# Optimization experiments

Hardware: AMD Instinct MI355X
Metric: run time of the kernel (lower is better)

## Reference

```python
import jax, jax.numpy as jnp
import numpy as np

NBITS = 1
GROUP_SIZE = 64
OUT_F = 4096
IN_F = 4096


def setup_inputs() -> dict:
    key = jax.random.key(0)
    k1, k2, k3, k4, k5 = jax.random.split(key, 5)
    x = jax.random.normal(k1, (8192, IN_F), dtype=jnp.float32)
    # packed 1-bit weights: 8 bits per byte, stored as int32 in [0,256)
    W_packed = jax.random.randint(k2, (OUT_F, IN_F // 8), 0, 256, dtype=jnp.int32)
    n_groups = OUT_F * IN_F // GROUP_SIZE
    scale = jax.random.uniform(k3, (n_groups, 1), dtype=jnp.float32) * 0.02 + 0.005
    zero = jax.random.normal(k4, (n_groups, 1), dtype=jnp.float32) * 0.5
    bias = jax.random.normal(k5, (OUT_F,), dtype=jnp.float32) * 0.02
    return {"x": x, "W_packed": W_packed, "scale": scale, "zero": zero, "bias": bias}


def _unpack_1bit(W_packed):
    # (out, in//8) int -> (out, in) float bits, bit 0 first within each byte
    bits = (W_packed[..., None] >> jnp.arange(8, dtype=jnp.int32)) & 1  # (out, in//8, 8)
    return bits.reshape(W_packed.shape[0], -1).astype(jnp.float32)      # (out, in)


def _dequantise(W_packed, scale, zero):
    W_q = _unpack_1bit(W_packed)                       # (out, in)
    W_grouped = W_q.reshape(-1, GROUP_SIZE)            # (n_groups, group_size), axis=1 grouping
    W_hat = (W_grouped - zero) * scale                 # per-group affine dequant
    return W_hat.reshape(OUT_F, IN_F)


def reference(x, W_packed, scale, zero, bias):
    W_hat = _dequantise(W_packed, scale, zero)
    # F.linear: x @ W_hat.T + bias
    return jnp.dot(x, W_hat.T) + bias
```

## Files before the change

### kernel.cpp

```cpp
#include <hip/hip_runtime.h>
#include <hip/hip_bf16.h>

#define IN_F   4096
#define OUT_F  4096
#define BK     64
#define NTILES (IN_F / BK)

typedef __bf16 bf16;
typedef __attribute__((ext_vector_type(8)))  __bf16 bf16x8;
typedef __attribute__((ext_vector_type(4)))  __bf16 bf16x4;
typedef __attribute__((ext_vector_type(4)))  float  floatx4;

__global__ __launch_bounds__(256) void prep_kernel(
    const float* __restrict__ x,  bf16* __restrict__ xb,
    const int* __restrict__ Wp,   const float* __restrict__ scale,
    const float* __restrict__ zero, bf16* __restrict__ Wb,
    int nx8, int nw)
{
    const int tid0   = (int)blockIdx.x * 256 + (int)threadIdx.x;
    const int stride = (int)gridDim.x * 256;

    for (int i = tid0; i < nx8; i += stride) {
        const float4 v0 = ((const float4*)x)[2 * (size_t)i];
        const float4 v1 = ((const float4*)x)[2 * (size_t)i + 1];
        bf16x8 b;
        b[0] = (bf16)v0.x; b[1] = (bf16)v0.y; b[2] = (bf16)v0.z; b[3] = (bf16)v0.w;
        b[4] = (bf16)v1.x; b[5] = (bf16)v1.y; b[6] = (bf16)v1.z; b[7] = (bf16)v1.w;
        ((bf16x8*)xb)[i] = b;
    }

    for (int i = tid0; i < nw; i += stride) {
        const int b = i & 511;
        const int g = ((i >> 9) << 6) + (b >> 3);
        const float sc = scale[g];
        const float zp = zero[g];
        const bf16 hi = (bf16)((1.0f - zp) * sc);
        const bf16 lo = (bf16)((0.0f - zp) * sc);
        const int v = Wp[i];
        bf16x8 w;
#pragma unroll
        for (int j = 0; j < 8; ++j) w[j] = ((v >> j) & 1) ? hi : lo;
        *(bf16x8*)&Wb[(size_t)i * 8] = w;
    }
}

__device__ __forceinline__ void gload_lds16(const void* g, void* l) {
    __builtin_amdgcn_global_load_lds(
        (const __attribute__((address_space(1))) unsigned int*)g,
        (__attribute__((address_space(3))) unsigned int*)l, 16, 0, 0);
}

#define CFENCE asm volatile("" ::: "memory")
#define SBAR() do { CFENCE; __builtin_amdgcn_s_barrier(); CFENCE; } while (0)
#define WAIT_LGKM0 asm volatile("s_waitcnt lgkmcnt(0)" ::: "memory")

#define STAGE(src, ldsTile, q, row0, kti) do {                                 \
    const int r_  = (q) * 64 + wave * 8 + srow;                                \
    const int gu_ = sun ^ (r_ & 7);                                            \
    gload_lds16((src) + (size_t)((row0) + r_) * IN_F + (kti) * BK + gu_ * 8,   \
                (ldsTile) + ((q) * 64 + wave * 8) * BK);                       \
} while (0)

#define LDFRAG(tile, row, u) \
    (*(const bf16x8*)((tile) + (row) * BK + (((u) ^ ((row) & 7)) << 3)))

#define LOAD_A(tile, MS)                                                       \
    _Pragma("unroll")                                                          \
    for (int i = 0; i < 4; ++i)                                                \
        _Pragma("unroll")                                                      \
        for (int ks = 0; ks < 2; ++ks)                                         \
            af[i][ks] = LDFRAG((tile), wm * 128 + (MS) * 64 + i * 16 + l15,    \
                               ks * 4 + l4);

#define LOAD_B_TO(dst, tile, NS)                                               \
    _Pragma("unroll")                                                          \
    for (int j = 0; j < 2; ++j)                                                \
        _Pragma("unroll")                                                      \
        for (int ks = 0; ks < 2; ++ks)                                         \
            dst[j][ks] = LDFRAG((tile), wn * 64 + (NS) * 32 + j * 16 + l15,    \
                                ks * 4 + l4);

#define MFMA_QUAD(AI, BJ, BFR)                                                 \
    __builtin_amdgcn_s_setprio(1);                                             \
    _Pragma("unroll")                                                          \
    for (int i = 0; i < 4; ++i)                                                \
        _Pragma("unroll")                                                      \
        for (int j = 0; j < 2; ++j)                                            \
            _Pragma("unroll")                                                  \
            for (int ks = 0; ks < 2; ++ks)                                     \
                acc[(AI) + i][(BJ) + j] =                                      \
                    __builtin_amdgcn_mfma_f32_16x16x32_bf16(                   \
                        af[i][ks], BFR[j][ks], acc[(AI) + i][(BJ) + j], 0, 0, 0); \
    __builtin_amdgcn_s_setprio(0);

__global__ __launch_bounds__(512, 2) void gemm256_8phase_kernel(
    const bf16* __restrict__ A,
    const bf16* __restrict__ B,
    const float* __restrict__ bias,
    float* __restrict__ out)
{
    __shared__ __align__(16) bf16 as_[2][256 * BK];
    __shared__ __align__(16) bf16 bs_[2][256 * BK];

    const int t    = threadIdx.x;
    const int lane = t & 63;
    const int wave = t >> 6;
    const int wm   = wave >> 2;
    const int wn   = wave & 3;
    const int l15  = lane & 15;
    const int l4   = lane >> 4;
    const int srow = lane >> 3;
    const int sun  = lane & 7;

    const int nwg = (int)gridDim.x;
    const int cpx = nwg >> 3;
    const int wg  = ((int)blockIdx.x & 7) * cpx + ((int)blockIdx.x >> 3);
    const int n0  = (wg & 15) * 256;
    const int m0  = (wg >> 4) * 256;

    floatx4 acc[8][4];
#pragma unroll
    for (int f = 0; f < 8; ++f)
#pragma unroll
        for (int g = 0; g < 4; ++g) acc[f][g] = (floatx4){0.f, 0.f, 0.f, 0.f};

#pragma unroll
    for (int q = 0; q < 4; ++q) STAGE(A, &as_[0][0], q, m0, 0);
#pragma unroll
    for (int q = 0; q < 4; ++q) STAGE(B, &bs_[0][0], q, n0, 0);
    STAGE(A, &as_[1][0], 0, m0, 1);
    STAGE(A, &as_[1][0], 2, m0, 1);
    asm volatile("s_waitcnt vmcnt(2)" ::: "memory");
    SBAR();

    bf16x8 af[4][2], bf0[2][2], bf1[2][2];

    for (int kt = 0; kt < NTILES; ++kt) {
        bf16* const At = &as_[kt & 1][0];
        bf16* const Bt = &bs_[kt & 1][0];
        bf16* const An = &as_[(kt & 1) ^ 1][0];
        bf16* const Bn = &bs_[(kt & 1) ^ 1][0];
        const int s1 = (kt + 1 < NTILES);
        const int s2 = (kt + 2 < NTILES);

        LOAD_A(At, 0);
        LOAD_B_TO(bf0, Bt, 0);
        if (s1) { STAGE(B, Bn, 0, n0, kt + 1); STAGE(B, Bn, 1, n0, kt + 1); }
        SBAR(); WAIT_LGKM0;
        MFMA_QUAD(0, 0, bf0);
        SBAR();

        LOAD_B_TO(bf1, Bt, 1);
        if (s1) { STAGE(B, Bn, 2, n0, kt + 1); STAGE(B, Bn, 3, n0, kt + 1); }
        SBAR(); WAIT_LGKM0;
        MFMA_QUAD(0, 2, bf1);
        if (s1) { asm volatile("s_waitcnt vmcnt(6)" ::: "memory"); }
        else    { asm volatile("s_waitcnt vmcnt(0)" ::: "memory"); }
        SBAR();

        LOAD_A(At, 1);
        if (s1) { STAGE(A, An, 1, m0, kt + 1); STAGE(A, An, 3, m0, kt + 1); }
        SBAR(); WAIT_LGKM0;
        MFMA_QUAD(4, 0, bf0);
        SBAR();

        if (s2) { STAGE(A, At, 0, m0, kt + 2); STAGE(A, At, 2, m0, kt + 2); }
        MFMA_QUAD(4, 2, bf1);
        if (s2) { asm volatile("s_waitcnt vmcnt(4)" ::: "memory"); }
        else    { asm volatile("s_waitcnt vmcnt(2)" ::: "memory"); }
        SBAR();
    }

#pragma unroll
    for (int g = 0; g < 4; ++g) {
        const int col = n0 + wn * 64 + g * 16 + l15;
        const float bv = bias[col];
#pragma unroll
        for (int f = 0; f < 8; ++f) {
            const int row = m0 + wm * 128 + f * 16 + l4 * 4;
#pragma unroll
            for (int r = 0; r < 4; ++r)
                out[(size_t)(row + r) * OUT_F + col] = acc[f][g][r] + bv;
        }
    }
}

#define SA 72
#define SB 72
__global__ __launch_bounds__(256) void hqq_gemm_fused_kernel(
    const float* __restrict__ x, const int* __restrict__ Wp,
    const float* __restrict__ scale, const float* __restrict__ zero,
    const float* __restrict__ bias, float* __restrict__ out)
{
    __shared__ __align__(16) bf16 asmem[128 * SA];
    __shared__ __align__(16) bf16 bsmem[128 * SB];
    const int t = threadIdx.x, lane = t & 63, wave = t >> 6;
    const int lane16 = lane & 15, kq = lane >> 4;
    const int wm = wave >> 1, wn = wave & 1;
    const int n0 = blockIdx.x * 128, m0 = blockIdx.y * 128;
    floatx4 acc[4][4];
#pragma unroll
    for (int i = 0; i < 4; ++i)
#pragma unroll
        for (int j = 0; j < 4; ++j) acc[i][j] = (floatx4){0.f, 0.f, 0.f, 0.f};
    const int a_col4 = t & 15, a_row0 = t >> 4;
    const int b_nl = t >> 1, b_half = t & 1;
    for (int kt = 0; kt < IN_F / 64; ++kt) {
        const float* xp = x + (size_t)(m0 + a_row0) * IN_F + kt * 64 + a_col4 * 4;
#pragma unroll
        for (int p = 0; p < 8; ++p) {
            float4 v = *(const float4*)(xp + (size_t)(p * 16) * IN_F);
            bf16x4 b = { (bf16)v.x, (bf16)v.y, (bf16)v.z, (bf16)v.w };
            *(bf16x4*)&asmem[(a_row0 + p * 16) * SA + a_col4 * 4] = b;
        }
        {
            const int4 v = *(const int4*)(Wp + (size_t)(n0 + b_nl) * (IN_F / 8)
                                          + kt * 8 + b_half * 4);
            const int g = (n0 + b_nl) * (IN_F / 64) + kt;
            const float sc = scale[g], zp = zero[g];
            const bf16 hi = (bf16)((1.0f - zp) * sc), lo = (bf16)(0.0f - zp * sc);
            const int vals[4] = {v.x, v.y, v.z, v.w};
#pragma unroll
            for (int e = 0; e < 4; ++e) {
                bf16x8 w;
#pragma unroll
                for (int j = 0; j < 8; ++j) w[j] = ((vals[e] >> j) & 1) ? hi : lo;
                *(bf16x8*)&bsmem[b_nl * SB + b_half * 32 + e * 8] = w;
            }
        }
        __syncthreads();
#pragma unroll
        for (int ks = 0; ks < 2; ++ks) {
            bf16x8 af[4], bfr[4];
#pragma unroll
            for (int i = 0; i < 4; ++i)
                af[i] = *(const bf16x8*)&asmem[(wm * 64 + i * 16 + lane16) * SA + ks * 32 + kq * 8];
#pragma unroll
            for (int j = 0; j < 4; ++j)
                bfr[j] = *(const bf16x8*)&bsmem[(wn * 64 + j * 16 + lane16) * SB + ks * 32 + kq * 8];
#pragma unroll
            for (int i = 0; i < 4; ++i)
#pragma unroll
                for (int j = 0; j < 4; ++j)
                    acc[i][j] = __builtin_amdgcn_mfma_f32_16x16x32_bf16(af[i], bfr[j], acc[i][j], 0, 0, 0);
        }
        __syncthreads();
    }
#pragma unroll
    for (int j = 0; j < 4; ++j) {
        const int col = n0 + wn * 64 + j * 16 + lane16;
        const float bv = bias[col];
#pragma unroll
        for (int i = 0; i < 4; ++i) {
            const int row = m0 + wm * 64 + i * 16 + kq * 4;
#pragma unroll
            for (int r = 0; r < 4; ++r)
                out[(size_t)(row + r) * OUT_F + col] = acc[i][j][r] + bv;
        }
    }
}

extern "C" void kernel_launch(void* const* d_in, const int* in_sizes, int n_in,
                              void* d_out, int out_size, void* d_ws, size_t ws_size,
                              hipStream_t stream) {
    const float* x     = (const float*)d_in[0];
    const int*   Wp    = (const int*)d_in[1];
    const float* scale = (const float*)d_in[2];
    const float* zero  = (const float*)d_in[3];
    const float* bias  = (const float*)d_in[4];
    float*       out   = (float*)d_out;

    const int M = in_sizes[0] / IN_F;
    const size_t need = (size_t)M * IN_F * 2 + (size_t)OUT_F * IN_F * 2;

    if (ws_size >= need && (M % 256) == 0) {
        bf16* xb = (bf16*)d_ws;
        bf16* Wb = (bf16*)((char*)d_ws + (size_t)M * IN_F * 2);

        const int nx8 = M * IN_F / 8;
        const int nw  = OUT_F * (IN_F / 8);
        prep_kernel<<<2048, 256, 0, stream>>>(x, xb, Wp, scale, zero, Wb, nx8, nw);

        gemm256_8phase_kernel<<<dim3((OUT_F / 256) * (M / 256)), 512, 0, stream>>>(
            xb, Wb, bias, out);
    } else {
        dim3 grid(OUT_F / 128, M / 128);
        hqq_gemm_fused_kernel<<<grid, 256, 0, stream>>>(x, Wp, scale, zero, bias, out);
    }
}
```

Measured before the change: 475.5 us.

## Fuse x conversion and weight dequant into the 256x256 GEMM main loop

```diff
diff --git a/kernel.cpp b/kernel.cpp
--- a/kernel.cpp
+++ b/kernel.cpp
@@ -11,54 +11,61 @@
 typedef __attribute__((ext_vector_type(4)))  __bf16 bf16x4;
 typedef __attribute__((ext_vector_type(4)))  float  floatx4;
 
-__global__ __launch_bounds__(256) void prep_kernel(
-    const float* __restrict__ x,  bf16* __restrict__ xb,
-    const int* __restrict__ Wp,   const float* __restrict__ scale,
-    const float* __restrict__ zero, bf16* __restrict__ Wb,
-    int nx8, int nw)
-{
-    const int tid0   = (int)blockIdx.x * 256 + (int)threadIdx.x;
-    const int stride = (int)gridDim.x * 256;
-
-    for (int i = tid0; i < nx8; i += stride) {
-        const float4 v0 = ((const float4*)x)[2 * (size_t)i];
-        const float4 v1 = ((const float4*)x)[2 * (size_t)i + 1];
-        bf16x8 b;
-        b[0] = (bf16)v0.x; b[1] = (bf16)v0.y; b[2] = (bf16)v0.z; b[3] = (bf16)v0.w;
-        b[4] = (bf16)v1.x; b[5] = (bf16)v1.y; b[6] = (bf16)v1.z; b[7] = (bf16)v1.w;
-        ((bf16x8*)xb)[i] = b;
-    }
-
-    for (int i = tid0; i < nw; i += stride) {
-        const int b = i & 511;
-        const int g = ((i >> 9) << 6) + (b >> 3);
-        const float sc = scale[g];
-        const float zp = zero[g];
-        const bf16 hi = (bf16)((1.0f - zp) * sc);
-        const bf16 lo = (bf16)((0.0f - zp) * sc);
-        const int v = Wp[i];
-        bf16x8 w;
-#pragma unroll
-        for (int j = 0; j < 8; ++j) w[j] = ((v >> j) & 1) ? hi : lo;
-        *(bf16x8*)&Wb[(size_t)i * 8] = w;
-    }
-}
-
-__device__ __forceinline__ void gload_lds16(const void* g, void* l) {
-    __builtin_amdgcn_global_load_lds(
-        (const __attribute__((address_space(1))) unsigned int*)g,
-        (__attribute__((address_space(3))) unsigned int*)l, 16, 0, 0);
-}
 
 #define CFENCE asm volatile("" ::: "memory")
 #define SBAR() do { CFENCE; __builtin_amdgcn_s_barrier(); CFENCE; } while (0)
 #define WAIT_LGKM0 asm volatile("s_waitcnt lgkmcnt(0)" ::: "memory")
 
-#define STAGE(src, ldsTile, q, row0, kti) do {                                 \
-    const int r_  = (q) * 64 + wave * 8 + srow;                                \
-    const int gu_ = sun ^ (r_ & 7);                                            \
-    gload_lds16((src) + (size_t)((row0) + r_) * IN_F + (kti) * BK + gu_ * 8,   \
-                (ldsTile) + ((q) * 64 + wave * 8) * BK);                       \
+#define LD_A2(nm, qa, qb, kti) do {                                            \
+    const int rA_ = (qa) * 64 + wave * 8 + srow;                               \
+    const int rB_ = (qb) * 64 + wave * 8 + srow;                               \
+    const float* pA_ = X + (size_t)(m0 + rA_) * IN_F + (kti) * BK + gu * 8;    \
+    const float* pB_ = X + (size_t)(m0 + rB_) * IN_F + (kti) * BK + gu * 8;    \
+    nm##_00 = *(const float4*)pA_;  nm##_01 = *(const float4*)(pA_ + 4);       \
+    nm##_10 = *(const float4*)pB_;  nm##_11 = *(const float4*)(pB_ + 4);       \
+} while (0)
+
+#define WR_A2(nm, qa, qb, buf) do {                                            \
+    const int rA_ = (qa) * 64 + wave * 8 + srow;                               \
+    const int rB_ = (qb) * 64 + wave * 8 + srow;                               \
+    bf16x8 vA_, vB_;                                                           \
+    vA_[0]=(bf16)nm##_00.x; vA_[1]=(bf16)nm##_00.y;                            \
+    vA_[2]=(bf16)nm##_00.z; vA_[3]=(bf16)nm##_00.w;                            \
+    vA_[4]=(bf16)nm##_01.x; vA_[5]=(bf16)nm##_01.y;                            \
+    vA_[6]=(bf16)nm##_01.z; vA_[7]=(bf16)nm##_01.w;                            \
+    vB_[0]=(bf16)nm##_10.x; vB_[1]=(bf16)nm##_10.y;                            \
+    vB_[2]=(bf16)nm##_10.z; vB_[3]=(bf16)nm##_10.w;                            \
+    vB_[4]=(bf16)nm##_11.x; vB_[5]=(bf16)nm##_11.y;                            \
+    vB_[6]=(bf16)nm##_11.z; vB_[7]=(bf16)nm##_11.w;                            \
+    *(bf16x8*)&(buf)[rA_ * BK + sun * 8] = vA_;                                \
+    *(bf16x8*)&(buf)[rB_ * BK + sun * 8] = vB_;                                \
+} while (0)
+
+#define LD_B2(nm, qa, qb, kti) do {                                            \
+    const int rA_ = (qa) * 64 + wave * 8 + srow;                               \
+    const int rB_ = (qb) * 64 + wave * 8 + srow;                               \
+    nm##_w0 = Wp[(size_t)(n0 + rA_) * (IN_F / 8) + (kti) * 8 + gu];            \
+    nm##_s0 = scale[(n0 + rA_) * (IN_F / 64) + (kti)];                         \
+    nm##_z0 = zero [(n0 + rA_) * (IN_F / 64) + (kti)];                         \
+    nm##_w1 = Wp[(size_t)(n0 + rB_) * (IN_F / 8) + (kti) * 8 + gu];            \
+    nm##_s1 = scale[(n0 + rB_) * (IN_F / 64) + (kti)];                         \
+    nm##_z1 = zero [(n0 + rB_) * (IN_F / 64) + (kti)];                         \
+} while (0)
+
+#define WR_B2(nm, qa, qb, buf) do {                                            \
+    const int rA_ = (qa) * 64 + wave * 8 + srow;                               \
+    const int rB_ = (qb) * 64 + wave * 8 + srow;                               \
+    const bf16 hA_ = (bf16)((1.0f - nm##_z0) * nm##_s0);                       \
+    const bf16 lA_ = (bf16)(0.0f - nm##_z0 * nm##_s0);                         \
+    const bf16 hB_ = (bf16)((1.0f - nm##_z1) * nm##_s1);                       \
+    const bf16 lB_ = (bf16)(0.0f - nm##_z1 * nm##_s1);                         \
+    bf16x8 vA_, vB_;                                                           \
+    _Pragma("unroll")                                                          \
+    for (int j_ = 0; j_ < 8; ++j_) vA_[j_] = ((nm##_w0 >> j_) & 1) ? hA_ : lA_;\
+    _Pragma("unroll")                                                          \
+    for (int j_ = 0; j_ < 8; ++j_) vB_[j_] = ((nm##_w1 >> j_) & 1) ? hB_ : lB_;\
+    *(bf16x8*)&(buf)[rA_ * BK + sun * 8] = vA_;                                \
+    *(bf16x8*)&(buf)[rB_ * BK + sun * 8] = vB_;                                \
 } while (0)
 
 #define LDFRAG(tile, row, u) \
@@ -93,11 +100,13 @@
                         af[i][ks], BFR[j][ks], acc[(AI) + i][(BJ) + j], 0, 0, 0); \
     __builtin_amdgcn_s_setprio(0);
 
-__global__ __launch_bounds__(512, 2) void gemm256_8phase_kernel(
-    const bf16* __restrict__ A,
-    const bf16* __restrict__ B,
+__global__ __launch_bounds__(512, 2) void hqq_fused256_kernel(
+    const float* __restrict__ X,
+    const int*   __restrict__ Wp,
+    const float* __restrict__ scale,
+    const float* __restrict__ zero,
     const float* __restrict__ bias,
-    float* __restrict__ out)
+    float*       __restrict__ out)
 {
     __shared__ __align__(16) bf16 as_[2][256 * BK];
     __shared__ __align__(16) bf16 bs_[2][256 * BK];
@@ -111,6 +120,7 @@
     const int l4   = lane >> 4;
     const int srow = lane >> 3;
     const int sun  = lane & 7;
+    const int gu   = sun ^ srow;
 
     const int nwg = (int)gridDim.x;
     const int cpx = nwg >> 3;
@@ -124,13 +134,25 @@
 #pragma unroll
         for (int g = 0; g < 4; ++g) acc[f][g] = (floatx4){0.f, 0.f, 0.f, 0.f};
 
-#pragma unroll
-    for (int q = 0; q < 4; ++q) STAGE(A, &as_[0][0], q, m0, 0);
-#pragma unroll
-    for (int q = 0; q < 4; ++q) STAGE(B, &bs_[0][0], q, n0, 0);
-    STAGE(A, &as_[1][0], 0, m0, 1);
-    STAGE(A, &as_[1][0], 2, m0, 1);
-    asm volatile("s_waitcnt vmcnt(2)" ::: "memory");
+    float4 aq02_00, aq02_01, aq02_10, aq02_11;
+    float4 aq13_00, aq13_01, aq13_10, aq13_11;
+    int   bq01_w0, bq01_w1;  float bq01_s0, bq01_z0, bq01_s1, bq01_z1;
+    int   bq23_w0, bq23_w1;  float bq23_s0, bq23_z0, bq23_s1, bq23_z1;
+
+    LD_A2(aq02, 0, 2, 0);
+    asm volatile("s_waitcnt vmcnt(0)" ::: "memory");
+    WR_A2(aq02, 0, 2, &as_[0][0]);
+    LD_A2(aq13, 1, 3, 0);
+    asm volatile("s_waitcnt vmcnt(0)" ::: "memory");
+    WR_A2(aq13, 1, 3, &as_[0][0]);
+    LD_B2(bq01, 0, 1, 0);
+    asm volatile("s_waitcnt vmcnt(0)" ::: "memory");
+    WR_B2(bq01, 0, 1, &bs_[0][0]);
+    LD_B2(bq23, 2, 3, 0);
+    asm volatile("s_waitcnt vmcnt(0)" ::: "memory");
+    WR_B2(bq23, 2, 3, &bs_[0][0]);
+    LD_A2(aq02, 0, 2, 1);
+    WAIT_LGKM0;
     SBAR();
 
     bf16x8 af[4][2], bf0[2][2], bf1[2][2];
@@ -145,29 +167,43 @@
 
         LOAD_A(At, 0);
         LOAD_B_TO(bf0, Bt, 0);
-        if (s1) { STAGE(B, Bn, 0, n0, kt + 1); STAGE(B, Bn, 1, n0, kt + 1); }
+        if (s1) {
+            LD_B2(bq01, 0, 1, kt + 1);
+            asm volatile("s_waitcnt vmcnt(6)" ::: "memory");
+            WR_A2(aq02, 0, 2, An);
+        }
         SBAR(); WAIT_LGKM0;
         MFMA_QUAD(0, 0, bf0);
         SBAR();
 
         LOAD_B_TO(bf1, Bt, 1);
-        if (s1) { STAGE(B, Bn, 2, n0, kt + 1); STAGE(B, Bn, 3, n0, kt + 1); }
+        if (s1) {
+            LD_B2(bq23, 2, 3, kt + 1);
+            asm volatile("s_waitcnt vmcnt(6)" ::: "memory");
+            WR_B2(bq01, 0, 1, Bn);
+        }
         SBAR(); WAIT_LGKM0;
         MFMA_QUAD(0, 2, bf1);
-        if (s1) { asm volatile("s_waitcnt vmcnt(6)" ::: "memory"); }
-        else    { asm volatile("s_waitcnt vmcnt(0)" ::: "memory"); }
         SBAR();
 
         LOAD_A(At, 1);
-        if (s1) { STAGE(A, An, 1, m0, kt + 1); STAGE(A, An, 3, m0, kt + 1); }
+        if (s1) {
+            LD_A2(aq13, 1, 3, kt + 1);
+            asm volatile("s_waitcnt vmcnt(4)" ::: "memory");
+            WR_B2(bq23, 2, 3, Bn);
+        }
         SBAR(); WAIT_LGKM0;
         MFMA_QUAD(4, 0, bf0);
         SBAR();
 
-        if (s2) { STAGE(A, At, 0, m0, kt + 2); STAGE(A, At, 2, m0, kt + 2); }
+        if (s2) LD_A2(aq02, 0, 2, kt + 2);
+        if (s1) {
+            if (s2) { asm volatile("s_waitcnt vmcnt(4)" ::: "memory"); }
+            else    { asm volatile("s_waitcnt vmcnt(0)" ::: "memory"); }
+            WR_A2(aq13, 1, 3, An);
+        }
         MFMA_QUAD(4, 2, bf1);
-        if (s2) { asm volatile("s_waitcnt vmcnt(4)" ::: "memory"); }
-        else    { asm volatile("s_waitcnt vmcnt(2)" ::: "memory"); }
+        WAIT_LGKM0;
         SBAR();
     }
 
@@ -271,18 +307,10 @@
     float*       out   = (float*)d_out;
 
     const int M = in_sizes[0] / IN_F;
-    const size_t need = (size_t)M * IN_F * 2 + (size_t)OUT_F * IN_F * 2;
-
-    if (ws_size >= need && (M % 256) == 0) {
-        bf16* xb = (bf16*)d_ws;
-        bf16* Wb = (bf16*)((char*)d_ws + (size_t)M * IN_F * 2);
-
-        const int nx8 = M * IN_F / 8;
-        const int nw  = OUT_F * (IN_F / 8);
-        prep_kernel<<<2048, 256, 0, stream>>>(x, xb, Wp, scale, zero, Wb, nx8, nw);
-
-        gemm256_8phase_kernel<<<dim3((OUT_F / 256) * (M / 256)), 512, 0, stream>>>(
-            xb, Wb, bias, out);
+
+    if ((M % 256) == 0) {
+        hqq_fused256_kernel<<<dim3((OUT_F / 256) * (M / 256)), 512, 0, stream>>>(
+            x, Wp, scale, zero, bias, out);
     } else {
         dim3 grid(OUT_F / 128, M / 128);
         hqq_gemm_fused_kernel<<<grid, 256, 0, stream>>>(x, Wp, scale, zero, bias, out);
```

New measurement: 669.3 us. +40.8%, slower.
